# Optimization experiments

Measured on AMD Instinct MI355X. Metric: run time of the kernel, lower is better.

## Reference

```python
import jax, jax.numpy as jnp
import numpy as np

B, H, T, D = 2, 16, 2048, 64


def setup_inputs() -> dict:
    key = jax.random.key(0)
    kq, kk, kv = jax.random.split(key, 3)
    Q = jax.random.normal(kq, (B, H, T, D), dtype=jnp.float32)
    K = jax.random.normal(kk, (B, H, T, D), dtype=jnp.float32)
    V = jax.random.normal(kv, (B, H, T, D), dtype=jnp.float32)
    return {"Q": Q, "K": K, "V": V}


def reference(Q, K, V):
    # Q,K,V: [B,H,T,D]; causal self-attention with 1/sqrt(D) temperature.
    Bq, Hq, Tq, Dq = Q.shape
    temperature = jnp.asarray(Dq, Q.dtype) ** 0.5
    # [B,H,T,T] attention scores
    scores = jnp.einsum('bhqd,bhkd->bhqk', Q, K) / temperature
    causal = jnp.tril(jnp.ones((Tq, Tq), dtype=bool))  # [T,T]
    scores = jnp.where(causal[None, None, :, :], scores, jnp.finfo(Q.dtype).min)
    weights = jax.nn.softmax(scores, axis=-1)
    return jnp.einsum('bhqk,bhkd->bhqd', weights, V)
```

## Files before the change

kernel.cpp:

```cpp
#include <hip/hip_runtime.h>
#include <hip/hip_bf16.h>
#include <math.h>


#define BATCH 2
#define HEADS 16
#define SEQ   2048
#define DIM   64
#define NBH   (BATCH * HEADS)
#define NKT_G (SEQ / 64)
#define TILE_SHORTS 4096

typedef __attribute__((ext_vector_type(8)))  short    bf16x8;
typedef __attribute__((ext_vector_type(4)))  unsigned u32x4;
typedef __attribute__((ext_vector_type(4)))  float    f32x4;
typedef __attribute__((ext_vector_type(16))) float    f32x16;

__device__ inline short f2bf(float f) {
    unsigned u = __builtin_bit_cast(unsigned, f);
    u += 0x7fff + ((u >> 16) & 1);
    return (short)(u >> 16);
}

__device__ inline unsigned cvtpk(float a, float b) {
    unsigned r;
    asm("v_cvt_pk_bf16_f32 %0, %1, %2" : "=v"(r) : "v"(a), "v"(b));
    return r;
}

__global__ __launch_bounds__(256)
void prep_kv(const float* __restrict__ K, const float* __restrict__ V,
             short* __restrict__ Kimg, short* __restrict__ Vimg) {
    const int tile = blockIdx.x;
    const int tid  = threadIdx.x;
    const float* Ksrc = K + (size_t)tile * TILE_SHORTS;
    const float* Vsrc = V + (size_t)tile * TILE_SHORTS;
    char* Kdst = (char*)(Kimg + (size_t)tile * TILE_SHORTS);
    char* Vdst = (char*)(Vimg + (size_t)tile * TILE_SHORTS);

    __shared__ float vt[64][65];

    {
        const int r  = tid >> 2;
        const int c0 = (tid & 3) * 16;
        #pragma unroll
        for (int j = 0; j < 16; j += 4) {
            const f32x4 v = *reinterpret_cast<const f32x4*>(Vsrc + (size_t)r * 64 + c0 + j);
            vt[r][c0+j] = v[0]; vt[r][c0+j+1] = v[1]; vt[r][c0+j+2] = v[2]; vt[r][c0+j+3] = v[3];
        }
    }

    const int f = tid >> 6;
    const int l = tid & 63;
    const int l31 = l & 31;
    const int l8  = (l >> 5) * 8;

    #pragma unroll
    for (int kb = 0; kb < 2; ++kb) {
        const float* src = Ksrc + (size_t)(kb * 32 + l31) * 64 + f * 16 + l8;
        const f32x4 a = *reinterpret_cast<const f32x4*>(src);
        const f32x4 b = *reinterpret_cast<const f32x4*>(src + 4);
        short h[8];
        #pragma unroll
        for (int j = 0; j < 4; ++j) { h[j] = f2bf(a[j]); h[4+j] = f2bf(b[j]); }
        *reinterpret_cast<bf16x8*>(Kdst + ((kb * 4 + f) * 64 + l) * 16) =
            *reinterpret_cast<bf16x8*>(h);
    }

    __syncthreads();

    #pragma unroll
    for (int db = 0; db < 2; ++db) {
        const int d  = db * 32 + l31;
        const int k0 = f * 16 + l8;
        short h[8];
        #pragma unroll
        for (int j = 0; j < 8; ++j) h[j] = f2bf(vt[k0 + j][d]);
        *reinterpret_cast<bf16x8*>(Vdst + ((db * 4 + f) * 64 + l) * 16) =
            *reinterpret_cast<bf16x8*>(h);
    }
}

__global__ __launch_bounds__(128)
void fa_fwd(const float* __restrict__ Q, const short* __restrict__ Kimg,
            const short* __restrict__ Vimg, float* __restrict__ O) {
    const int tid  = threadIdx.x;
    const int lane = tid & 63;
    const int wid  = tid >> 6;
    const int q31  = lane & 31;
    const int hi2  = lane >> 5;

    const int idx = blockIdx.x;
    const int m   = idx >> 5;
    const int bh  = idx & 31;
    const int qm  = (m < 16) ? (31 - m) : (m - 16);
    const int qw  = qm * 64 + wid * 32;
    const int nkt = qm + 1;

    const float* Qb = Q + (size_t)bh * SEQ * DIM;
    float*       Ob = O + (size_t)bh * SEQ * DIM;
    const char*  Ktb = (const char*)(Kimg + (size_t)bh * NKT_G * TILE_SHORTS);
    const char*  Vtb = (const char*)(Vimg + (size_t)bh * NKT_G * TILE_SHORTS);
    const unsigned lb = (unsigned)lane * 16;

    const float SCL = 0.18033688011112042f;
    bf16x8 qf[4];
    #pragma unroll
    for (int ds = 0; ds < 4; ++ds) {
        const float* src = Qb + (size_t)(qw + q31) * DIM + ds * 16 + hi2 * 8;
        const f32x4 a = *reinterpret_cast<const f32x4*>(src);
        const f32x4 b = *reinterpret_cast<const f32x4*>(src + 4);
        bf16x8 q;
        #pragma unroll
        for (int jj = 0; jj < 4; ++jj) {
            q[jj]     = f2bf(a[jj] * SCL);
            q[4 + jj] = f2bf(b[jj] * SCL);
        }
        qf[ds] = q;
    }

    f32x16 acc0 = {}, acc1 = {};
    float rs = 0.f;
    const int qrel = wid * 32 + q31;

    for (int kt = 0; kt < nkt; ++kt) {
        const char* Kt = Ktb + (size_t)kt * 8192;
        const char* Vt = Vtb + (size_t)kt * 8192;

        bf16x8 kf[2][4], vf[2][4];
        #pragma unroll
        for (int kb = 0; kb < 2; ++kb)
            #pragma unroll
            for (int ds = 0; ds < 4; ++ds)
                kf[kb][ds] = *reinterpret_cast<const bf16x8*>(
                    Kt + (kb * 4 + ds) * 1024 + lb);
        #pragma unroll
        for (int db = 0; db < 2; ++db)
            #pragma unroll
            for (int s = 0; s < 4; ++s)
                vf[db][s] = *reinterpret_cast<const bf16x8*>(
                    Vt + (db * 4 + s) * 1024 + lb);

        f32x16 st0 = {}, st1 = {};
        __builtin_amdgcn_s_setprio(1);
        #pragma unroll
        for (int ds = 0; ds < 4; ++ds)
            st0 = __builtin_amdgcn_mfma_f32_32x32x16_bf16(kf[0][ds], qf[ds], st0, 0, 0, 0);
        #pragma unroll
        for (int ds = 0; ds < 4; ++ds)
            st1 = __builtin_amdgcn_mfma_f32_32x32x16_bf16(kf[1][ds], qf[ds], st1, 0, 0, 0);
        __builtin_amdgcn_s_setprio(0);

        const bool lastt = (kt == nkt - 1);
        float p0[16], p1[16];
        #pragma unroll
        for (int r = 0; r < 16; ++r) {
            const int kloc = (r & 3) + 8 * (r >> 2) + 4 * hi2;
            float v0 = __builtin_amdgcn_exp2f(st0[r]);
            float v1 = __builtin_amdgcn_exp2f(st1[r]);
            if (lastt) {
                if (kloc > qrel)      v0 = 0.f;
                if (kloc + 32 > qrel) v1 = 0.f;
            }
            p0[r] = v0; p1[r] = v1;
            rs += v0 + v1;
        }

        __builtin_amdgcn_s_setprio(1);
        #pragma unroll
        for (int s = 0; s < 4; ++s) {
            const float* pk = (s >> 1) ? p1 : p0;
            const int u = (s & 1) * 8;
            unsigned Xa = cvtpk(pk[u],     pk[u + 1]);
            unsigned Ya = cvtpk(pk[u + 2], pk[u + 3]);
            unsigned Xb = cvtpk(pk[u + 4], pk[u + 5]);
            unsigned Yb = cvtpk(pk[u + 6], pk[u + 7]);
            asm("v_permlane32_swap_b32 %0, %1" : "+v"(Xa), "+v"(Xb));
            asm("v_permlane32_swap_b32 %0, %1" : "+v"(Ya), "+v"(Yb));
            const u32x4 w = {Xa, Ya, Xb, Yb};
            const bf16x8 pa = __builtin_bit_cast(bf16x8, w);
            acc0 = __builtin_amdgcn_mfma_f32_32x32x16_bf16(pa, vf[0][s], acc0, 0, 0, 0);
            acc1 = __builtin_amdgcn_mfma_f32_32x32x16_bf16(pa, vf[1][s], acc1, 0, 0, 0);
        }
        __builtin_amdgcn_s_setprio(0);
    }

    rs += __shfl_xor(rs, 32, 64);
    const float inv = 1.0f / rs;
    #pragma unroll
    for (int r = 0; r < 16; ++r) {
        const int off = (r & 3) + 8 * (r >> 2) + 4 * hi2;
        const float ir = __shfl(inv, off, 64);
        float* dst = Ob + (size_t)(qw + off) * DIM + q31;
        dst[0]  = acc0[r] * ir;
        dst[32] = acc1[r] * ir;
    }
}

extern "C" void kernel_launch(void* const* d_in, const int* in_sizes, int n_in,
                              void* d_out, int out_size, void* d_ws, size_t ws_size,
                              hipStream_t stream) {
    const float* Q = (const float*)d_in[0];
    const float* K = (const float*)d_in[1];
    const float* V = (const float*)d_in[2];
    float*       O = (float*)d_out;

    short* Kimg = (short*)d_ws;
    short* Vimg = (short*)d_ws + (size_t)NBH * NKT_G * TILE_SHORTS;

    prep_kv<<<dim3(NBH * NKT_G), dim3(256), 0, stream>>>(K, V, Kimg, Vimg);
    fa_fwd<<<dim3(NBH * 32), dim3(128), 0, stream>>>(Q, Kimg, Vimg, O);
}
```

Baseline: 49.45 us.

## Split KV range across two waves per 32-row query block with LDS reduction

Each block now handles a single 32-row query block instead of 64 rows. Its two waves take alternating KV tiles and merge their partial accumulators and row sums through shared memory before writing the output. The grid doubles, blocks are ordered in a serpentine pattern over query position to balance causal work, and launch bounds now request 4 blocks per CU. The aim is more parallelism and better load balance across CUs. The cost is an LDS reduction and barrier per block, and each K/V tile is now read by twice as many blocks in total.

```diff
diff --git a/kernel.cpp b/kernel.cpp
--- a/kernel.cpp
+++ b/kernel.cpp
@@ -81,7 +81,7 @@
     }
 }
 
-__global__ __launch_bounds__(128)
+__global__ __launch_bounds__(128, 4)
 void fa_fwd(const float* __restrict__ Q, const short* __restrict__ Kimg,
             const short* __restrict__ Vimg, float* __restrict__ O) {
     const int tid  = threadIdx.x;
@@ -91,17 +91,23 @@
     const int hi2  = lane >> 5;
 
     const int idx = blockIdx.x;
-    const int m   = idx >> 5;
     const int bh  = idx & 31;
-    const int qm  = (m < 16) ? (31 - m) : (m - 16);
-    const int qw  = qm * 64 + wid * 32;
-    const int nkt = qm + 1;
+    const int j   = idx >> 5;
+    const int k8  = j >> 3;
+    const int g8  = j & 7;
+    const int p   = (k8 & 1) ? (k8 * 8 + 7 - g8) : j;
+    const int qw  = p * 32;
+    const int kd  = p >> 1;
+    const int qrel = (p & 1) * 32 + q31;
 
     const float* Qb = Q + (size_t)bh * SEQ * DIM;
     float*       Ob = O + (size_t)bh * SEQ * DIM;
     const char*  Ktb = (const char*)(Kimg + (size_t)bh * NKT_G * TILE_SHORTS);
     const char*  Vtb = (const char*)(Vimg + (size_t)bh * NKT_G * TILE_SHORTS);
     const unsigned lb = (unsigned)lane * 16;
+
+    __shared__ float accL[32][64];
+    __shared__ float rsL[32];
 
     const float SCL = 0.18033688011112042f;
     bf16x8 qf[4];
@@ -121,9 +127,8 @@
 
     f32x16 acc0 = {}, acc1 = {};
     float rs = 0.f;
-    const int qrel = wid * 32 + q31;
-
-    for (int kt = 0; kt < nkt; ++kt) {
+
+    for (int kt = wid; kt <= kd; kt += 2) {
         const char* Kt = Ktb + (size_t)kt * 8192;
         const char* Vt = Vtb + (size_t)kt * 8192;
 
@@ -151,7 +156,7 @@
             st1 = __builtin_amdgcn_mfma_f32_32x32x16_bf16(kf[1][ds], qf[ds], st1, 0, 0, 0);
         __builtin_amdgcn_s_setprio(0);
 
-        const bool lastt = (kt == nkt - 1);
+        const bool lastt = (kt == kd);
         float p0[16], p1[16];
         #pragma unroll
         for (int r = 0; r < 16; ++r) {
@@ -186,14 +191,31 @@
     }
 
     rs += __shfl_xor(rs, 32, 64);
-    const float inv = 1.0f / rs;
-    #pragma unroll
-    for (int r = 0; r < 16; ++r) {
-        const int off = (r & 3) + 8 * (r >> 2) + 4 * hi2;
-        const float ir = __shfl(inv, off, 64);
-        float* dst = Ob + (size_t)(qw + off) * DIM + q31;
-        dst[0]  = acc0[r] * ir;
-        dst[32] = acc1[r] * ir;
+
+    if (wid == 0) {
+        #pragma unroll
+        for (int r = 0; r < 16; ++r) {
+            const int off = (r & 3) + 8 * (r >> 2) + 4 * hi2;
+            accL[off][q31]      = acc0[r];
+            accL[off][q31 + 32] = acc1[r];
+        }
+        if (lane < 32) rsL[lane] = rs;
+    }
+    __syncthreads();
+
+    if (wid == 1) {
+        const float rstot = rs + rsL[q31];
+        const float inv = 1.0f / rstot;
+        #pragma unroll
+        for (int r = 0; r < 16; ++r) {
+            const int off = (r & 3) + 8 * (r >> 2) + 4 * hi2;
+            const float ir = __shfl(inv, off, 64);
+            const float o0 = acc0[r] + accL[off][q31];
+            const float o1 = acc1[r] + accL[off][q31 + 32];
+            float* dst = Ob + (size_t)(qw + off) * DIM + q31;
+            dst[0]  = o0 * ir;
+            dst[32] = o1 * ir;
+        }
     }
 }
 
@@ -209,5 +231,5 @@
     short* Vimg = (short*)d_ws + (size_t)NBH * NKT_G * TILE_SHORTS;
 
     prep_kv<<<dim3(NBH * NKT_G), dim3(256), 0, stream>>>(K, V, Kimg, Vimg);
-    fa_fwd<<<dim3(NBH * 32), dim3(128), 0, stream>>>(Q, Kimg, Vimg, O);
-}
+    fa_fwd<<<dim3(NBH * 64), dim3(128), 0, stream>>>(Q, Kimg, Vimg, O);
+}
```

Measured after the change: 72.73 us. 47.1% more time.

## Share K tiles across four waves via async LDS double buffering

Applied to the files above, without the earlier changes.

Each block now covers 128 query rows with four waves instead of 64 rows with two. K tiles are staged once per block into a double-buffered LDS ring using global_load_lds, and all four waves read K from there, while V is still loaded straight from global memory. The goal is to cut redundant K traffic from global memory and L2 and to overlap the next tile's load with the current compute. The cost is a block-wide barrier every iteration, waves that sit idle once they pass their own causal diagonal, and half as many blocks.

```diff
diff --git a/kernel.cpp b/kernel.cpp
--- a/kernel.cpp
+++ b/kernel.cpp
@@ -26,6 +26,12 @@
     unsigned r;
     asm("v_cvt_pk_bf16_f32 %0, %1, %2" : "=v"(r) : "v"(a), "v"(b));
     return r;
+}
+
+__device__ inline void gload16(const void* g, void* l) {
+    __builtin_amdgcn_global_load_lds(
+        (const __attribute__((address_space(1))) unsigned*)g,
+        (__attribute__((address_space(3))) unsigned*)l, 16, 0, 0);
 }
 
 __global__ __launch_bounds__(256)
@@ -81,21 +87,24 @@
     }
 }
 
-__global__ __launch_bounds__(128)
+__global__ __launch_bounds__(256)
 void fa_fwd(const float* __restrict__ Q, const short* __restrict__ Kimg,
             const short* __restrict__ Vimg, float* __restrict__ O) {
     const int tid  = threadIdx.x;
     const int lane = tid & 63;
-    const int wid  = tid >> 6;
+    const int w    = tid >> 6;
     const int q31  = lane & 31;
     const int hi2  = lane >> 5;
 
     const int idx = blockIdx.x;
-    const int m   = idx >> 5;
     const int bh  = idx & 31;
-    const int qm  = (m < 16) ? (31 - m) : (m - 16);
-    const int qw  = qm * 64 + wid * 32;
-    const int nkt = qm + 1;
+    const int jj  = idx >> 5;
+    const int qt  = (jj < 8) ? jj : (23 - jj);
+    const int q0  = qt * 128;
+    const int qw  = q0 + w * 32;
+    const int nkt = 2 * qt + 2;
+    const int kd  = 2 * qt + (w >> 1);
+    const int qrel = (w & 1) * 32 + q31;
 
     const float* Qb = Q + (size_t)bh * SEQ * DIM;
     float*       Ob = O + (size_t)bh * SEQ * DIM;
@@ -103,6 +112,15 @@
     const char*  Vtb = (const char*)(Vimg + (size_t)bh * NKT_G * TILE_SHORTS);
     const unsigned lb = (unsigned)lane * 16;
 
+    __shared__ short Klds[2][TILE_SHORTS];
+
+    auto stage = [&](int bb, int kt) {
+        const char* Kt = Ktb + (size_t)kt * 8192;
+        char* Lb = (char*)Klds[bb] + (unsigned)w * 1024;
+        gload16(Kt + (unsigned)w * 1024 + lb,        Lb);
+        gload16(Kt + 4096 + (unsigned)w * 1024 + lb, (char*)Lb + 4096);
+    };
+
     const float SCL = 0.18033688011112042f;
     bf16x8 qf[4];
     #pragma unroll
@@ -112,77 +130,87 @@
         const f32x4 b = *reinterpret_cast<const f32x4*>(src + 4);
         bf16x8 q;
         #pragma unroll
-        for (int jj = 0; jj < 4; ++jj) {
-            q[jj]     = f2bf(a[jj] * SCL);
-            q[4 + jj] = f2bf(b[jj] * SCL);
+        for (int jx = 0; jx < 4; ++jx) {
+            q[jx]     = f2bf(a[jx] * SCL);
+            q[4 + jx] = f2bf(b[jx] * SCL);
         }
         qf[ds] = q;
     }
 
     f32x16 acc0 = {}, acc1 = {};
     float rs = 0.f;
-    const int qrel = wid * 32 + q31;
+
+    stage(0, 0);
+    __syncthreads();
 
     for (int kt = 0; kt < nkt; ++kt) {
-        const char* Kt = Ktb + (size_t)kt * 8192;
-        const char* Vt = Vtb + (size_t)kt * 8192;
-
-        bf16x8 kf[2][4], vf[2][4];
-        #pragma unroll
-        for (int kb = 0; kb < 2; ++kb)
+        const int bb = kt & 1;
+        if (kt + 1 < nkt) stage(bb ^ 1, kt + 1);
+
+        if (kt <= kd) {
+            const char* Vt = Vtb + (size_t)kt * 8192;
+            bf16x8 vf[2][4];
+            #pragma unroll
+            for (int db = 0; db < 2; ++db)
+                #pragma unroll
+                for (int s = 0; s < 4; ++s)
+                    vf[db][s] = *reinterpret_cast<const bf16x8*>(
+                        Vt + (db * 4 + s) * 1024 + lb);
+
+            const char* Kb = (const char*)Klds[bb];
+            bf16x8 kf[2][4];
+            #pragma unroll
+            for (int kb = 0; kb < 2; ++kb)
+                #pragma unroll
+                for (int ds = 0; ds < 4; ++ds)
+                    kf[kb][ds] = *reinterpret_cast<const bf16x8*>(
+                        Kb + (kb * 4 + ds) * 1024 + lb);
+
+            f32x16 st0 = {}, st1 = {};
+            __builtin_amdgcn_s_setprio(1);
             #pragma unroll
             for (int ds = 0; ds < 4; ++ds)
-                kf[kb][ds] = *reinterpret_cast<const bf16x8*>(
-                    Kt + (kb * 4 + ds) * 1024 + lb);
-        #pragma unroll
-        for (int db = 0; db < 2; ++db)
-            #pragma unroll
-            for (int s = 0; s < 4; ++s)
-                vf[db][s] = *reinterpret_cast<const bf16x8*>(
-                    Vt + (db * 4 + s) * 1024 + lb);
-
-        f32x16 st0 = {}, st1 = {};
-        __builtin_amdgcn_s_setprio(1);
-        #pragma unroll
-        for (int ds = 0; ds < 4; ++ds)
-            st0 = __builtin_amdgcn_mfma_f32_32x32x16_bf16(kf[0][ds], qf[ds], st0, 0, 0, 0);
-        #pragma unroll
-        for (int ds = 0; ds < 4; ++ds)
-            st1 = __builtin_amdgcn_mfma_f32_32x32x16_bf16(kf[1][ds], qf[ds], st1, 0, 0, 0);
-        __builtin_amdgcn_s_setprio(0);
-
-        const bool lastt = (kt == nkt - 1);
-        float p0[16], p1[16];
-        #pragma unroll
-        for (int r = 0; r < 16; ++r) {
-            const int kloc = (r & 3) + 8 * (r >> 2) + 4 * hi2;
-            float v0 = __builtin_amdgcn_exp2f(st0[r]);
-            float v1 = __builtin_amdgcn_exp2f(st1[r]);
-            if (lastt) {
-                if (kloc > qrel)      v0 = 0.f;
-                if (kloc + 32 > qrel) v1 = 0.f;
+                st0 = __builtin_amdgcn_mfma_f32_32x32x16_bf16(kf[0][ds], qf[ds], st0, 0, 0, 0);
+            #pragma unroll
+            for (int ds = 0; ds < 4; ++ds)
+                st1 = __builtin_amdgcn_mfma_f32_32x32x16_bf16(kf[1][ds], qf[ds], st1, 0, 0, 0);
+            __builtin_amdgcn_s_setprio(0);
+
+            const bool lastt = (kt == kd);
+            float p0[16], p1[16];
+            #pragma unroll
+            for (int r = 0; r < 16; ++r) {
+                const int kloc = (r & 3) + 8 * (r >> 2) + 4 * hi2;
+                float v0 = __builtin_amdgcn_exp2f(st0[r]);
+                float v1 = __builtin_amdgcn_exp2f(st1[r]);
+                if (lastt) {
+                    if (kloc > qrel)      v0 = 0.f;
+                    if (kloc + 32 > qrel) v1 = 0.f;
+                }
+                p0[r] = v0; p1[r] = v1;
+                rs += v0 + v1;
             }
-            p0[r] = v0; p1[r] = v1;
-            rs += v0 + v1;
+
+            __builtin_amdgcn_s_setprio(1);
+            #pragma unroll
+            for (int s = 0; s < 4; ++s) {
+                const float* pk = (s >> 1) ? p1 : p0;
+                const int u = (s & 1) * 8;
+                unsigned Xa = cvtpk(pk[u],     pk[u + 1]);
+                unsigned Ya = cvtpk(pk[u + 2], pk[u + 3]);
+                unsigned Xb = cvtpk(pk[u + 4], pk[u + 5]);
+                unsigned Yb = cvtpk(pk[u + 6], pk[u + 7]);
+                asm("v_permlane32_swap_b32 %0, %1" : "+v"(Xa), "+v"(Xb));
+                asm("v_permlane32_swap_b32 %0, %1" : "+v"(Ya), "+v"(Yb));
+                const u32x4 ww = {Xa, Ya, Xb, Yb};
+                const bf16x8 pa = __builtin_bit_cast(bf16x8, ww);
+                acc0 = __builtin_amdgcn_mfma_f32_32x32x16_bf16(pa, vf[0][s], acc0, 0, 0, 0);
+                acc1 = __builtin_amdgcn_mfma_f32_32x32x16_bf16(pa, vf[1][s], acc1, 0, 0, 0);
+            }
+            __builtin_amdgcn_s_setprio(0);
         }
 
-        __builtin_amdgcn_s_setprio(1);
-        #pragma unroll
-        for (int s = 0; s < 4; ++s) {
-            const float* pk = (s >> 1) ? p1 : p0;
-            const int u = (s & 1) * 8;
-            unsigned Xa = cvtpk(pk[u],     pk[u + 1]);
-            unsigned Ya = cvtpk(pk[u + 2], pk[u + 3]);
-            unsigned Xb = cvtpk(pk[u + 4], pk[u + 5]);
-            unsigned Yb = cvtpk(pk[u + 6], pk[u + 7]);
-            asm("v_permlane32_swap_b32 %0, %1" : "+v"(Xa), "+v"(Xb));
-            asm("v_permlane32_swap_b32 %0, %1" : "+v"(Ya), "+v"(Yb));
-            const u32x4 w = {Xa, Ya, Xb, Yb};
-            const bf16x8 pa = __builtin_bit_cast(bf16x8, w);
-            acc0 = __builtin_amdgcn_mfma_f32_32x32x16_bf16(pa, vf[0][s], acc0, 0, 0, 0);
-            acc1 = __builtin_amdgcn_mfma_f32_32x32x16_bf16(pa, vf[1][s], acc1, 0, 0, 0);
-        }
-        __builtin_amdgcn_s_setprio(0);
+        __syncthreads();
     }
 
     rs += __shfl_xor(rs, 32, 64);
@@ -209,5 +237,5 @@
     short* Vimg = (short*)d_ws + (size_t)NBH * NKT_G * TILE_SHORTS;
 
     prep_kv<<<dim3(NBH * NKT_G), dim3(256), 0, stream>>>(K, V, Kimg, Vimg);
-    fa_fwd<<<dim3(NBH * 32), dim3(128), 0, stream>>>(Q, Kimg, Vimg, O);
-}
+    fa_fwd<<<dim3(NBH * 16), dim3(256), 0, stream>>>(Q, Kimg, Vimg, O);
+}
```

New measurement: 54.75 us. 10.7% more time.
